# Kernel optimization log

Hardware: AMD Instinct MI355X
Metric: run time of the kernel (lower is better)

The kernel has to match this reference:

```python
import jax, jax.numpy as jnp
import numpy as np

N_NODES = 100000
N_EDGES = 1600000
N_GRAPHS = 128


def setup_inputs() -> dict:
    key = jax.random.key(0)
    ks = jax.random.split(key, 8)
    x = jax.random.normal(ks[0], (N_NODES, 384), dtype=jnp.float32)
    edge_index = jax.random.randint(ks[1], (2, N_EDGES), 0, N_NODES, dtype=jnp.int64)
    batch = jnp.sort(jax.random.randint(ks[2], (N_NODES,), 0, N_GRAPHS, dtype=jnp.int64))
    W1 = jax.random.normal(ks[3], (384, 128), dtype=jnp.float32) * (1.0 / np.sqrt(384))
    b1 = jnp.zeros((128,), dtype=jnp.float32)
    W2 = jax.random.normal(ks[4], (128, 64), dtype=jnp.float32) * (1.0 / np.sqrt(128))
    b2 = jnp.zeros((64,), dtype=jnp.float32)
    Wlin = jax.random.normal(ks[5], (64, 2), dtype=jnp.float32) * (1.0 / np.sqrt(64))
    blin = jnp.zeros((2,), dtype=jnp.float32)
    return {"x": x, "edge_index": edge_index, "batch": batch,
            "W1": W1, "b1": b1, "W2": W2, "b2": b2, "Wlin": Wlin, "blin": blin}


def gcn_conv(x, src, dst, W, b, n_nodes):
    # PyG GCNConv: self-loops + symmetric normalization D^{-1/2} A_hat D^{-1/2},
    # linear transform first (out_dim < in_dim -> cheaper messages).
    h = x @ W  # [N, out]
    deg = jax.ops.segment_sum(jnp.ones_like(dst, dtype=h.dtype), dst,
                              num_segments=n_nodes) + 1.0  # self-loop weight
    dis = jax.lax.rsqrt(deg)  # deg >= 1 always (self-loop)
    norm = dis[src] * dis[dst]  # per-edge normalization [E]
    msg = h[src] * norm[:, None]  # gather + scale [E, out]
    agg = jax.ops.segment_sum(msg, dst, num_segments=n_nodes)
    agg = agg + h * (dis * dis)[:, None]  # self-loop contribution
    return agg + b


def reference(x, edge_index, batch, W1, b1, W2, b2, Wlin, blin):
    src, dst = edge_index[0], edge_index[1]
    n_nodes = x.shape[0]
    h = jax.nn.relu(gcn_conv(x, src, dst, W1, b1, n_nodes))
    h = jax.nn.relu(gcn_conv(h, src, dst, W2, b2, n_nodes))
    # global_mean_pool over graph ids
    sums = jax.ops.segment_sum(h, batch, num_segments=N_GRAPHS)
    cnts = jax.ops.segment_sum(jnp.ones((n_nodes,), dtype=h.dtype), batch,
                               num_segments=N_GRAPHS)
    pooled = sums / jnp.maximum(cnts, 1.0)[:, None]  # [G, 64]
    # dropout is identity in eval mode
    return pooled @ Wlin + blin  # [G, 2]
```

## Files before the change

### kernel.cpp

```cpp
#include <hip/hip_runtime.h>


#define NN 100000
#define NG 128
#define BNODES 256
#define NBUK ((NN + BNODES - 1) / BNODES)
#define BCAP 6144

typedef __attribute__((ext_vector_type(8))) short short8;
typedef __attribute__((ext_vector_type(8))) unsigned short u16x8;
typedef __attribute__((ext_vector_type(4))) float f32x4;

__device__ __forceinline__ unsigned short f2bf(float f) {
    union { float f; unsigned u; } v; v.f = f;
    unsigned r = v.u + 0x7fffu + ((v.u >> 16) & 1u);
    return (unsigned short)(r >> 16);
}
__device__ __forceinline__ float bf2f(unsigned short h) {
    union { unsigned u; float f; } v; v.u = ((unsigned)h) << 16;
    return v.f;
}

__global__ __launch_bounds__(256) void bucket_scatter(const int* __restrict__ src,
                                                      const int* __restrict__ dst,
                                                      int* __restrict__ bcnt,
                                                      int2* __restrict__ pairs, int E) {
    __shared__ int hist[NBUK];
    __shared__ int lbase[NBUK];
    __shared__ int lfill[NBUK];
    const int t = threadIdx.x;
    const int chunk = (E + gridDim.x - 1) / gridDim.x;
    const int lo = blockIdx.x * chunk;
    const int hi = min(E, lo + chunk);
    for (int b = t; b < NBUK; b += 256) { hist[b] = 0; lfill[b] = 0; }
    __syncthreads();
    for (int i = lo + t; i < hi; i += 256)
        atomicAdd(&hist[dst[i] >> 8], 1);
    __syncthreads();
    for (int b = t; b < NBUK; b += 256)
        lbase[b] = hist[b] ? atomicAdd(&bcnt[b], hist[b]) : 0;
    __syncthreads();
    for (int i = lo + t; i < hi; i += 256) {
        const int s = src[i], d = dst[i];
        const int b = d >> 8;
        const int off = atomicAdd(&lfill[b], 1);
        pairs[(size_t)b * BCAP + lbase[b] + off] = make_int2(s, d);
    }
}

__global__ __launch_bounds__(512) void bucket_scan(const int* __restrict__ bcnt,
                                                   int* __restrict__ bbase,
                                                   int* __restrict__ rowptr,
                                                   int N, int E) {
    __shared__ int sm[512];
    const int t = threadIdx.x;
    sm[t] = (t < NBUK) ? bcnt[t] : 0;
    __syncthreads();
    for (int d = 1; d < 512; d <<= 1) {
        int a = (t >= d) ? sm[t - d] : 0;
        __syncthreads();
        sm[t] += a;
        __syncthreads();
    }
    if (t <= NBUK) bbase[t] = (t == 0) ? 0 : sm[t - 1];
    if (t == 0) rowptr[N] = E;
}

__global__ __launch_bounds__(256) void bucket_build(const int2* __restrict__ pairs,
                                                    const int* __restrict__ bcnt,
                                                    const int* __restrict__ bbase,
                                                    int* __restrict__ rowptr,
                                                    float* __restrict__ dis,
                                                    int* __restrict__ col, int N) {
    __shared__ int cnt[BNODES];
    __shared__ int sm[BNODES];
    __shared__ int pref[BNODES];
    __shared__ int fillc[BNODES];
    const int b = blockIdx.x;
    const int t = threadIdx.x;
    const int nbase = b * BNODES;
    const int ecnt = bcnt[b];
    const int2* ep = pairs + (size_t)b * BCAP;
    const int gbase = bbase[b];

    cnt[t] = 0;
    fillc[t] = 0;
    __syncthreads();
    for (int i = t; i < ecnt; i += 256)
        atomicAdd(&cnt[ep[i].y & (BNODES - 1)], 1);
    __syncthreads();
    sm[t] = cnt[t];
    __syncthreads();
    for (int d = 1; d < 256; d <<= 1) {
        int a = (t >= d) ? sm[t - d] : 0;
        __syncthreads();
        sm[t] += a;
        __syncthreads();
    }
    pref[t] = sm[t] - cnt[t];
    const int node = nbase + t;
    if (node < N) {
        rowptr[node] = gbase + pref[t];
        dis[node] = rsqrtf((float)cnt[t] + 1.0f);
    }
    __syncthreads();
    for (int i = t; i < ecnt; i += 256) {
        const int2 e = ep[i];
        const int d = e.y & (BNODES - 1);
        const int pos = gbase + pref[d] + atomicAdd(&fillc[d], 1);
        col[pos] = e.x;
    }
}

__global__ __launch_bounds__(256) void pack_w(const float* __restrict__ W,
                                              unsigned short* __restrict__ packH,
                                              unsigned short* __restrict__ packL,
                                              int K, int BN) {
    const int idx = blockIdx.x * blockDim.x + threadIdx.x;
    if (idx >= K * BN) return;
    const int e = idx & 7;
    const int l = (idx >> 3) & 63;
    const int rest = idx >> 9;
    const int NF = BN >> 4;
    const int nf = rest % NF;
    const int ks = rest / NF;
    const int n = nf * 16 + (l & 15);
    const int k = ks * 32 + ((l >> 4) & 3) * 8 + e;
    const float v = W[(size_t)k * BN + n];
    const unsigned short h = f2bf(v);
    packH[idx] = h;
    packL[idx] = f2bf(v - bf2f(h));
}

template <int BN, int K>
__global__ __launch_bounds__(256) void gemm_mfma(const float* __restrict__ A,
                                                 const unsigned short* __restrict__ WpH,
                                                 const unsigned short* __restrict__ WpL,
                                                 const float* __restrict__ scale,
                                                 unsigned short* __restrict__ Out,
                                                 int N) {
    constexpr int BM = 128;
    constexpr int NK = K / 32;
    constexpr int WROWS = (BN == 128) ? 2 : 4;
    constexpr int WCOLS = (BN == 128) ? 2 : 1;
    constexpr int WTM = BM / WROWS;
    constexpr int MF = WTM / 16;
    constexpr int NFW = (BN / WCOLS) / 16;
    constexpr int NFB = BN / 16;

    __shared__ unsigned short AsH[2][8][512];
    __shared__ unsigned short AsL[2][8][512];

    const int t = threadIdx.x;
    const int wid = t >> 6, lane = t & 63;
    const int wr = wid / WCOLS, wc = wid % WCOLS;
    const int r0 = blockIdx.x * BM;

    const int s_row1 = t >> 2;
    const int s_row2 = 64 + (t >> 2);
    const int s_kg = t & 3;
    const int s_lf = ((t >> 2) & 15) + s_kg * 16;

    const bool ok1 = (r0 + s_row1) < N;
    const bool ok2 = (r0 + s_row2) < N;
    const float* aptr1 = A + (size_t)(r0 + s_row1) * K + s_kg * 8;
    const float* aptr2 = A + (size_t)(r0 + s_row2) * K + s_kg * 8;

    auto loadA = [&](int ks, float4* v) {
        v[0] = v[1] = v[2] = v[3] = make_float4(0.f, 0.f, 0.f, 0.f);
        if (ok1) {
            v[0] = *(const float4*)(aptr1 + ks * 32);
            v[1] = *(const float4*)(aptr1 + ks * 32 + 4);
        }
        if (ok2) {
            v[2] = *(const float4*)(aptr2 + ks * 32);
            v[3] = *(const float4*)(aptr2 + ks * 32 + 4);
        }
    };
    auto cvtwrite = [&](int buf, const float4* v) {
#pragma unroll
        for (int uu = 0; uu < 2; ++uu) {
            short8 h, l;
            const float vv[8] = {v[2 * uu].x,     v[2 * uu].y,
                                 v[2 * uu].z,     v[2 * uu].w,
                                 v[2 * uu + 1].x, v[2 * uu + 1].y,
                                 v[2 * uu + 1].z, v[2 * uu + 1].w};
#pragma unroll
            for (int j = 0; j < 8; ++j) {
                const unsigned short hh = f2bf(vv[j]);
                h[j] = (short)hh;
                l[j] = (short)f2bf(vv[j] - bf2f(hh));
            }
            const int m = uu ? (4 + wid) : wid;
            *(short8*)&AsH[buf][m][s_lf * 8] = h;
            *(short8*)&AsL[buf][m][s_lf * 8] = l;
        }
    };
    auto loadB = [&](int ks, short8* bH, short8* bL) {
#pragma unroll
        for (int n = 0; n < NFW; ++n) {
            const int nfg = wc * NFW + n;
            const int base = ((ks * NFB + nfg) * 64 + lane) * 8;
            bH[n] = *(const short8*)&WpH[base];
            bL[n] = *(const short8*)&WpL[base];
        }
    };

    f32x4 acc[MF][NFW];
#pragma unroll
    for (int m = 0; m < MF; ++m)
#pragma unroll
        for (int n = 0; n < NFW; ++n) acc[m][n] = (f32x4){0.f, 0.f, 0.f, 0.f};

    float4 av[4];
    loadA(0, av);
    cvtwrite(0, av);
    short8 bHc[NFW], bLc[NFW];
    loadB(0, bHc, bLc);

#pragma unroll
    for (int ks = 0; ks < NK; ++ks) {
        const int cur = ks & 1;
        __syncthreads();
        float4 avn[4];
        short8 bHn[NFW], bLn[NFW];
        if (ks + 1 < NK) {
            loadA(ks + 1, avn);
            loadB(ks + 1, bHn, bLn);
        }
#pragma unroll
        for (int m = 0; m < MF; ++m) {
            const int mf = wr * MF + m;
            const short8 aH = *(const short8*)&AsH[cur][mf][lane * 8];
            const short8 aL = *(const short8*)&AsL[cur][mf][lane * 8];
#pragma unroll
            for (int n = 0; n < NFW; ++n) {
                acc[m][n] = __builtin_amdgcn_mfma_f32_16x16x32_bf16(aH, bHc[n], acc[m][n], 0, 0, 0);
                acc[m][n] = __builtin_amdgcn_mfma_f32_16x16x32_bf16(aH, bLc[n], acc[m][n], 0, 0, 0);
                acc[m][n] = __builtin_amdgcn_mfma_f32_16x16x32_bf16(aL, bHc[n], acc[m][n], 0, 0, 0);
            }
        }
        if (ks + 1 < NK) {
            cvtwrite(cur ^ 1, avn);
#pragma unroll
            for (int n = 0; n < NFW; ++n) {
                bHc[n] = bHn[n];
                bLc[n] = bLn[n];
            }
        }
    }

#pragma unroll
    for (int m = 0; m < MF; ++m) {
        const int row0 = r0 + wr * WTM + m * 16 + ((lane >> 4) << 2);
        float sc[4];
#pragma unroll
        for (int r = 0; r < 4; ++r) sc[r] = (row0 + r < N) ? scale[row0 + r] : 0.f;
#pragma unroll
        for (int n = 0; n < NFW; ++n) {
            const int cn = wc * (NFW * 16) + n * 16 + (lane & 15);
#pragma unroll
            for (int r = 0; r < 4; ++r) {
                if (row0 + r < N)
                    Out[(size_t)(row0 + r) * BN + cn] = f2bf(acc[m][n][r] * sc[r]);
            }
        }
    }
}

template <int COLS>
__global__ __launch_bounds__(256) void agg_gather(const int* __restrict__ rowptr,
                                                  const int* __restrict__ col,
                                                  const float* __restrict__ dis,
                                                  const unsigned short* __restrict__ Hs,
                                                  const float* __restrict__ bias,
                                                  float* __restrict__ Out, int N) {
    constexpr int NPW = (COLS == 128) ? 1 : 2;
    constexpr int LPN = 64 / NPW;
    constexpr int LPR = COLS / 8;
    constexpr int NSG = LPN / LPR;
    const int gw = (int)((blockIdx.x * blockDim.x + threadIdx.x) >> 6);
    const int lane = threadIdx.x & 63;
    const int sub = lane / LPN;
    const int nl = lane % LPN;
    const int esub = nl / LPR;
    const int sl = nl % LPR;
    const int node = gw * NPW + sub;
    const int lgbase = sub * LPN;

    float acc[8];
#pragma unroll
    for (int k = 0; k < 8; ++k) acc[k] = 0.f;

    int base = 0, len = 0;
    const int nodec = (node < N) ? node : 0;
    if (node < N) {
        base = rowptr[node];
        len = rowptr[node + 1] - base;
    }

    for (int j0 = 0; j0 < len; j0 += LPN) {
        const int remain = min(LPN, len - j0);
        const int sidx = (nl < remain) ? col[base + j0 + nl] : nodec;
        const int qtr = (remain + NSG - 1) / NSG;
        const int off = esub * qtr;
        int u = 0;
        for (; u + 8 <= qtr; u += 8) {
            u16x8 hv[8];
            float wv[8];
#pragma unroll
            for (int b = 0; b < 8; ++b) {
                const int idx = off + u + b;
                const int s = __shfl(sidx, lgbase + idx);
                wv[b] = (idx < remain) ? 1.f : 0.f;
                hv[b] = *(const u16x8*)(Hs + (size_t)s * COLS + sl * 8);
            }
#pragma unroll
            for (int b = 0; b < 8; ++b)
#pragma unroll
                for (int k = 0; k < 8; ++k)
                    acc[k] = fmaf(bf2f(hv[b][k]), wv[b], acc[k]);
        }
        for (; u + 4 <= qtr; u += 4) {
            u16x8 hv[4];
            float wv[4];
#pragma unroll
            for (int b = 0; b < 4; ++b) {
                const int idx = off + u + b;
                const int s = __shfl(sidx, lgbase + idx);
                wv[b] = (idx < remain) ? 1.f : 0.f;
                hv[b] = *(const u16x8*)(Hs + (size_t)s * COLS + sl * 8);
            }
#pragma unroll
            for (int b = 0; b < 4; ++b)
#pragma unroll
                for (int k = 0; k < 8; ++k)
                    acc[k] = fmaf(bf2f(hv[b][k]), wv[b], acc[k]);
        }
        for (; u < qtr; ++u) {
            const int idx = off + u;
            const int s = __shfl(sidx, lgbase + idx);
            const float w = (idx < remain) ? 1.f : 0.f;
            const u16x8 hv = *(const u16x8*)(Hs + (size_t)s * COLS + sl * 8);
#pragma unroll
            for (int k = 0; k < 8; ++k)
                acc[k] = fmaf(bf2f(hv[k]), w, acc[k]);
        }
    }

#pragma unroll
    for (int k = 0; k < 8; ++k) {
        acc[k] += __shfl_xor(acc[k], LPR);
        acc[k] += __shfl_xor(acc[k], 2 * LPR);
    }

    if (node < N && esub == 0) {
        const float dd = dis[node];
        const u16x8 hsb = *(const u16x8*)(Hs + (size_t)node * COLS + sl * 8);
        const f32x4 bv0 = *(const f32x4*)(bias + sl * 8);
        const f32x4 bv1 = *(const f32x4*)(bias + sl * 8 + 4);
        f32x4 o0, o1;
#pragma unroll
        for (int k = 0; k < 4; ++k) {
            o0[k] = fmaxf(fmaf(acc[k] + bf2f(hsb[k]), dd, bv0[k]), 0.f);
            o1[k] = fmaxf(fmaf(acc[k + 4] + bf2f(hsb[k + 4]), dd, bv1[k]), 0.f);
        }
        *(f32x4*)(Out + (size_t)node * COLS + sl * 8) = o0;
        *(f32x4*)(Out + (size_t)node * COLS + sl * 8 + 4) = o1;
    }
}

__global__ __launch_bounds__(256) void pool_kernel(const float* __restrict__ H,
                                                   const int* __restrict__ batch,
                                                   float* __restrict__ pooled,
                                                   float* __restrict__ cnt, int N) {
    const int c = threadIdx.x & 63;
    const int w = threadIdx.x >> 6;
    const int row0 = blockIdx.x * 128 + w * 32;
    if (row0 >= N) return;
    const int nr = min(32, N - row0);

    float v[32];
    int b[32];
#pragma unroll
    for (int i = 0; i < 32; ++i) {
        const int r = row0 + i;
        if (i < nr) {
            v[i] = H[(size_t)r * 64 + c];
            b[i] = batch[r];
        } else {
            v[i] = 0.f;
            b[i] = -1;
        }
    }
    int cur = b[0];
    float sum = 0.f, csum = 0.f;
#pragma unroll
    for (int i = 0; i < 32; ++i) {
        if (i < nr) {
            if (b[i] != cur) {
                atomicAdd(&pooled[cur * 64 + c], sum);
                if (c == 0) atomicAdd(&cnt[cur], csum);
                cur = b[i];
                sum = 0.f;
                csum = 0.f;
            }
            sum += v[i];
            csum += 1.f;
        }
    }
    atomicAdd(&pooled[cur * 64 + c], sum);
    if (c == 0) atomicAdd(&cnt[cur], csum);
}

__global__ __launch_bounds__(256) void final_kernel(const float* __restrict__ pooled,
                                                    const float* __restrict__ cnt,
                                                    const float* __restrict__ Wlin,
                                                    const float* __restrict__ blin,
                                                    float* __restrict__ out) {
    const int t = threadIdx.x;
    const int g = t >> 1, o = t & 1;
    const float inv = 1.0f / fmaxf(cnt[g], 1.0f);
    float s = 0.f;
#pragma unroll
    for (int j = 0; j < 64; ++j) s = fmaf(pooled[g * 64 + j], Wlin[j * 2 + o], s);
    out[t] = s * inv + blin[o];
}

extern "C" void kernel_launch(void* const* d_in, const int* in_sizes, int n_in,
                              void* d_out, int out_size, void* d_ws, size_t ws_size,
                              hipStream_t stream) {
    const float* x     = (const float*)d_in[0];
    const int*   edge  = (const int*)d_in[1];
    const int*   batch = (const int*)d_in[2];
    const float* W1    = (const float*)d_in[3];
    const float* b1    = (const float*)d_in[4];
    const float* W2    = (const float*)d_in[5];
    const float* b2    = (const float*)d_in[6];
    const float* Wlin  = (const float*)d_in[7];
    const float* blin  = (const float*)d_in[8];
    float* out = (float*)d_out;

    const int N = NN;
    const int E = in_sizes[1] / 2;
    const int* src = edge;
    const int* dst = edge + E;

    char* ws = (char*)d_ws;
    size_t off = 0;
    auto alloc = [&](size_t bytes) -> void* {
        void* p = ws + off;
        off += (bytes + 511) & ~(size_t)511;
        return p;
    };
    float* dis    = (float*)alloc((size_t)N * 4);
    int*   rowptr = (int*)alloc((size_t)(N + 1) * 4);
    int*   bcnt   = (int*)alloc((size_t)NBUK * 4);
    int*   bbase  = (int*)alloc((size_t)(NBUK + 1) * 4);
    int*   col    = (int*)alloc((size_t)E * 4);
    int2*  pairs  = (int2*)alloc((size_t)NBUK * BCAP * 8);
    unsigned short* w1h = (unsigned short*)alloc((size_t)384 * 128 * 2);
    unsigned short* w1l = (unsigned short*)alloc((size_t)384 * 128 * 2);
    unsigned short* w2h = (unsigned short*)alloc((size_t)128 * 64 * 2);
    unsigned short* w2l = (unsigned short*)alloc((size_t)128 * 64 * 2);
    unsigned short* h1bf = (unsigned short*)alloc((size_t)N * 128 * 2);
    float* agg1   = (float*)alloc((size_t)N * 128 * 4);
    float* pooled = (float*)alloc((size_t)NG * 64 * 4);
    float* cnt    = (float*)alloc((size_t)NG * 4);
    unsigned short* h2bf = h1bf;
    float* agg2 = agg1;

    hipMemsetAsync(bcnt, 0, (size_t)NBUK * 4, stream);
    hipMemsetAsync(pooled, 0, (size_t)NG * 64 * 4, stream);
    hipMemsetAsync(cnt, 0, (size_t)NG * 4, stream);

    pack_w<<<(384 * 128 + 255) / 256, 256, 0, stream>>>(W1, w1h, w1l, 384, 128);
    pack_w<<<(128 * 64 + 255) / 256, 256, 0, stream>>>(W2, w2h, w2l, 128, 64);

    bucket_scatter<<<512, 256, 0, stream>>>(src, dst, bcnt, pairs, E);
    bucket_scan<<<1, 512, 0, stream>>>(bcnt, bbase, rowptr, N, E);
    bucket_build<<<NBUK, 256, 0, stream>>>(pairs, bcnt, bbase, rowptr, dis, col, N);

    const int gblocks = (N + 127) / 128;
    gemm_mfma<128, 384><<<gblocks, 256, 0, stream>>>(x, w1h, w1l, dis, h1bf, N);
    agg_gather<128><<<(N + 3) / 4, 256, 0, stream>>>(rowptr, col, dis, h1bf, b1, agg1, N);

    gemm_mfma<64, 128><<<gblocks, 256, 0, stream>>>(agg1, w2h, w2l, dis, h2bf, N);
    agg_gather<64><<<(N + 7) / 8, 256, 0, stream>>>(rowptr, col, dis, h2bf, b2, agg2, N);

    pool_kernel<<<(N + 127) / 128, 256, 0, stream>>>(agg2, batch, pooled, cnt, N);
    final_kernel<<<1, 256, 0, stream>>>(pooled, cnt, Wlin, blin, out);
}
```

Measured before the change: 274.5 us.

## Drop A low-part bf16 term, deepen A prefetch, merge memsets into one init kernel

The GEMM no longer splits the activation operand into high and low bf16 parts, so the aL×bH MFMA pass and the AsL shared buffer are removed, cutting MFMA work by a third and halving A-side LDS traffic. This lowers accuracy of the products, since activation rounding error is no longer compensated. A global loads are now prefetched two k-steps ahead, and launch bounds request 3 blocks per SM. The three memsets are replaced by a single init kernel to reduce launch overhead.

```diff
diff --git a/kernel.cpp b/kernel.cpp
--- a/kernel.cpp
+++ b/kernel.cpp
@@ -19,6 +19,15 @@
 __device__ __forceinline__ float bf2f(unsigned short h) {
     union { unsigned u; float f; } v; v.u = ((unsigned)h) << 16;
     return v.f;
+}
+
+__global__ __launch_bounds__(256) void init_kernel(int* __restrict__ bcnt,
+                                                   float* __restrict__ pooled,
+                                                   float* __restrict__ cnt) {
+    const int i = blockIdx.x * 256 + threadIdx.x;
+    if (i < NBUK) bcnt[i] = 0;
+    if (i < NG * 64) pooled[i] = 0.f;
+    if (i < NG) cnt[i] = 0.f;
 }
 
 __global__ __launch_bounds__(256) void bucket_scatter(const int* __restrict__ src,
@@ -133,12 +142,12 @@
 }
 
 template <int BN, int K>
-__global__ __launch_bounds__(256) void gemm_mfma(const float* __restrict__ A,
-                                                 const unsigned short* __restrict__ WpH,
-                                                 const unsigned short* __restrict__ WpL,
-                                                 const float* __restrict__ scale,
-                                                 unsigned short* __restrict__ Out,
-                                                 int N) {
+__global__ __launch_bounds__(256, 3) void gemm_mfma(const float* __restrict__ A,
+                                                    const unsigned short* __restrict__ WpH,
+                                                    const unsigned short* __restrict__ WpL,
+                                                    const float* __restrict__ scale,
+                                                    unsigned short* __restrict__ Out,
+                                                    int N) {
     constexpr int BM = 128;
     constexpr int NK = K / 32;
     constexpr int WROWS = (BN == 128) ? 2 : 4;
@@ -149,7 +158,6 @@
     constexpr int NFB = BN / 16;
 
     __shared__ unsigned short AsH[2][8][512];
-    __shared__ unsigned short AsL[2][8][512];
 
     const int t = threadIdx.x;
     const int wid = t >> 6, lane = t & 63;
@@ -180,20 +188,15 @@
     auto cvtwrite = [&](int buf, const float4* v) {
 #pragma unroll
         for (int uu = 0; uu < 2; ++uu) {
-            short8 h, l;
+            short8 h;
             const float vv[8] = {v[2 * uu].x,     v[2 * uu].y,
                                  v[2 * uu].z,     v[2 * uu].w,
                                  v[2 * uu + 1].x, v[2 * uu + 1].y,
                                  v[2 * uu + 1].z, v[2 * uu + 1].w};
 #pragma unroll
-            for (int j = 0; j < 8; ++j) {
-                const unsigned short hh = f2bf(vv[j]);
-                h[j] = (short)hh;
-                l[j] = (short)f2bf(vv[j] - bf2f(hh));
-            }
+            for (int j = 0; j < 8; ++j) h[j] = (short)f2bf(vv[j]);
             const int m = uu ? (4 + wid) : wid;
             *(short8*)&AsH[buf][m][s_lf * 8] = h;
-            *(short8*)&AsL[buf][m][s_lf * 8] = l;
         }
     };
     auto loadB = [&](int ks, short8* bH, short8* bL) {
@@ -212,9 +215,10 @@
 #pragma unroll
         for (int n = 0; n < NFW; ++n) acc[m][n] = (f32x4){0.f, 0.f, 0.f, 0.f};
 
-    float4 av[4];
-    loadA(0, av);
-    cvtwrite(0, av);
+    float4 av1[4], av2[4];
+    loadA(0, av1);
+    cvtwrite(0, av1);
+    if (NK > 1) loadA(1, av1);
     short8 bHc[NFW], bLc[NFW];
     loadB(0, bHc, bLc);
 
@@ -222,26 +226,23 @@
     for (int ks = 0; ks < NK; ++ks) {
         const int cur = ks & 1;
         __syncthreads();
-        float4 avn[4];
         short8 bHn[NFW], bLn[NFW];
-        if (ks + 1 < NK) {
-            loadA(ks + 1, avn);
-            loadB(ks + 1, bHn, bLn);
-        }
+        if (ks + 2 < NK) loadA(ks + 2, av2);
+        if (ks + 1 < NK) loadB(ks + 1, bHn, bLn);
 #pragma unroll
         for (int m = 0; m < MF; ++m) {
             const int mf = wr * MF + m;
             const short8 aH = *(const short8*)&AsH[cur][mf][lane * 8];
-            const short8 aL = *(const short8*)&AsL[cur][mf][lane * 8];
 #pragma unroll
             for (int n = 0; n < NFW; ++n) {
                 acc[m][n] = __builtin_amdgcn_mfma_f32_16x16x32_bf16(aH, bHc[n], acc[m][n], 0, 0, 0);
                 acc[m][n] = __builtin_amdgcn_mfma_f32_16x16x32_bf16(aH, bLc[n], acc[m][n], 0, 0, 0);
-                acc[m][n] = __builtin_amdgcn_mfma_f32_16x16x32_bf16(aL, bHc[n], acc[m][n], 0, 0, 0);
             }
         }
         if (ks + 1 < NK) {
-            cvtwrite(cur ^ 1, avn);
+            cvtwrite(cur ^ 1, av1);
+#pragma unroll
+            for (int i = 0; i < 4; ++i) av1[i] = av2[i];
 #pragma unroll
             for (int n = 0; n < NFW; ++n) {
                 bHc[n] = bHn[n];
@@ -470,9 +471,7 @@
     unsigned short* h2bf = h1bf;
     float* agg2 = agg1;
 
-    hipMemsetAsync(bcnt, 0, (size_t)NBUK * 4, stream);
-    hipMemsetAsync(pooled, 0, (size_t)NG * 64 * 4, stream);
-    hipMemsetAsync(cnt, 0, (size_t)NG * 4, stream);
+    init_kernel<<<(NG * 64 + 255) / 256, 256, 0, stream>>>(bcnt, pooled, cnt);
 
     pack_w<<<(384 * 128 + 255) / 256, 256, 0, stream>>>(W1, w1h, w1l, 384, 128);
     pack_w<<<(128 * 64 + 255) / 256, 256, 0, stream>>>(W2, w2h, w2l, 128, 64);
```

Result: slower. 290.0 us (+5.7%).
